# Kernel optimization log

Measured on AMD Instinct MI355X. Metric: run time of the kernel, lower is better.

Reference implementation:

```python
import jax, jax.numpy as jnp
import numpy as np

B, S, IN, OUT = 16, 512, 512, 256
D, H, L, DFF = 1024, 16, 6, 2048
HD = D // H
SCALE = HD ** -0.5
HID = 256  # fc1/fc2 hidden size


def setup_inputs() -> dict:
    key = jax.random.key(0)
    ks = jax.random.split(key, 40)
    g = lambda i, shape, s=0.02: (jax.random.normal(ks[i], shape, jnp.float32) * s)
    z = lambda shape: jnp.zeros(shape, jnp.float32)
    o = lambda shape: jnp.ones(shape, jnp.float32)
    vec = jnp.zeros((B, S), jnp.int32).at[:, 0].set(1)  # one-hot rows (assert-only arg)
    return {
        "x": jax.random.normal(ks[0], (B, S, IN), jnp.float32),
        "xm": jax.random.uniform(ks[1], (B, S), jnp.float32),
        "vecSelector": vec,
        "proj_w": g(2, (IN, D)), "proj_b": z((D,)),
        "pos": g(3, (S, D)),
        "qw": g(4, (L, D, D)), "qb": z((L, D)),
        "kw": g(5, (L, D, D)), "kb": z((L, D)),
        "vw": g(6, (L, D, D)), "vb": z((L, D)),
        "ow": g(7, (L, D, D)), "ob": z((L, D)),
        "ln1_g": o((L, D)), "ln1_b": z((L, D)),
        "ln2_g": o((L, D)), "ln2_b": z((L, D)),
        "w1": g(8, (L, D, DFF)), "b1": z((L, DFF)),
        "w2": g(9, (L, DFF, D)), "b2": z((L, D)),
        "fc1_w": g(10, (D, HID)), "fc1_b": z((HID,)),
        "fc2_w": g(11, (HID, HID)), "fc2_b": z((HID,)),
        "fc3_w": g(12, (HID, OUT)), "fc3_b": z((OUT,)),
    }


def _ln(x, g, b, eps=1e-5):
    m = jnp.mean(x, -1, keepdims=True)
    v = jnp.mean((x - m) ** 2, -1, keepdims=True)
    return (x - m) * jax.lax.rsqrt(v + eps) * g + b


def reference(x, xm, vecSelector, proj_w, proj_b, pos, qw, qb, kw, kb, vw, vb,
              ow, ob, ln1_g, ln1_b, ln2_g, ln2_b, w1, b1, w2, b2,
              fc1_w, fc1_b, fc2_w, fc2_b, fc3_w, fc3_b):
    # linear_proj + positional encoding (pos[:, :d_model] == pos)
    h = x @ proj_w + proj_b + pos  # (B,S,D)
    # key padding mask: whole batch rows masked where xm.sum(-1)==0
    skpm = jnp.broadcast_to((jnp.sum(xm, -1) == 0)[:, None], (B, S))  # (B,S) bool
    neg_inf = jnp.float32(-jnp.inf)
    for i in range(L):
        q = (h @ qw[i] + qb[i]) * SCALE
        k = h @ kw[i] + kb[i]
        v = h @ vw[i] + vb[i]
        q = q.reshape(B, S, H, HD)
        k = k.reshape(B, S, H, HD)
        v = v.reshape(B, S, H, HD)
        sc = jnp.einsum('bthd,bshd->bhts', q, k)  # (B,H,T,S)
        sc = jnp.where(skpm[:, None, None, :], neg_inf, sc)
        # safe_softmax: clamp to [-10,10] THEN softmax (-inf -> -10)
        aw = jax.nn.softmax(jnp.clip(sc, -10.0, 10.0), axis=-1)
        ao = jnp.einsum('bhts,bshd->bthd', aw, v).reshape(B, S, D)
        ao = ao @ ow[i] + ob[i]
        # forward hook: clamp + softmax over embed dim
        ao = jax.nn.softmax(jnp.clip(ao, -10.0, 10.0), axis=-1)
        # torch _sa_block's `[0]` slices batch dim of the raw tensor -> (S,D),
        # broadcast-added to every batch row
        sa = ao[0]
        h = _ln(h + sa[None, :, :], ln1_g[i], ln1_b[i])
        ff = jax.nn.relu(h @ w1[i] + b1[i]) @ w2[i] + b2[i]
        h = _ln(h + ff, ln2_g[i], ln2_b[i])
    out = h @ fc1_w + fc1_b
    for _ in range(5):
        out = out @ fc2_w + fc2_b
    out = out @ fc3_w + fc3_b  # (B,S,OUT)
    return out
```

## Files before the change

### kernel.cpp

```cpp
#include <hip/hip_runtime.h>
#include <hip/hip_bf16.h>

using bf16 = __hip_bfloat16;
typedef __attribute__((ext_vector_type(8))) short short8v;
typedef __attribute__((ext_vector_type(4))) float floatx4;

constexpr int Bc = 16, Sc = 512, INc = 512, OUTc = 256;
constexpr int Dc = 1024, Hc = 16, Lc = 6, DFFc = 2048, HIDc = 256;
constexpr float SCALEc = 0.125f;
constexpr int QKVS = 3072;
constexpr size_t LSLOT = 8388608;

__device__ inline ushort f2b(float f) {
    union { float f; unsigned u; } v; v.f = f;
    unsigned r = (v.u + 0x7FFF + ((v.u >> 16) & 1)) >> 16;
    return (ushort)r;
}
__device__ inline float b2f(ushort b) {
    union { unsigned u; float f; } v; v.u = ((unsigned)b) << 16;
    return v.f;
}
__device__ inline float ldf(const float* p) { return *p; }
__device__ inline float ldf(const ushort* p) { return b2f(*p); }

__device__ inline void gll16(const ushort* g, ushort* l) {
    __builtin_amdgcn_global_load_lds(
        (const __attribute__((address_space(1))) unsigned int*)g,
        (__attribute__((address_space(3))) unsigned int*)l, 16, 0, 0);
}

__device__ inline float blockSum256(float v) {
    __shared__ float tmp[4];
#pragma unroll
    for (int o = 32; o > 0; o >>= 1) v += __shfl_xor(v, o, 64);
    int w = threadIdx.x >> 6;
    __syncthreads();
    if ((threadIdx.x & 63) == 0) tmp[w] = v;
    __syncthreads();
    return tmp[0] + tmp[1] + tmp[2] + tmp[3];
}
__device__ inline float blockMax256(float v) {
    __shared__ float tmp[4];
#pragma unroll
    for (int o = 32; o > 0; o >>= 1) v = fmaxf(v, __shfl_xor(v, o, 64));
    int w = threadIdx.x >> 6;
    __syncthreads();
    if ((threadIdx.x & 63) == 0) tmp[w] = v;
    __syncthreads();
    return fmaxf(fmaxf(tmp[0], tmp[1]), fmaxf(tmp[2], tmp[3]));
}

__global__ __launch_bounds__(256) void mask_k(const float* __restrict__ xm, float* __restrict__ flag) {
    float s = xm[threadIdx.x] + xm[threadIdx.x + 256];
    s = blockSum256(s);
    if (threadIdx.x == 0) flag[0] = (s == 0.f) ? 1.f : 0.f;
}

__global__ __launch_bounds__(256) void transp_k(const float* __restrict__ W, ushort* __restrict__ Wt,
                                                int K, int N, float wscale) {
    __shared__ float Ls[64][65];
    const int t = threadIdx.x;
    const int n0 = blockIdx.x * 64, k0 = blockIdx.y * 64;
    const int kr = t >> 4, n4 = (t & 15) * 4;
#pragma unroll
    for (int p = 0; p < 4; ++p) {
        float4 v = *(const float4*)&W[(size_t)(k0 + kr + p * 16) * N + n0 + n4];
        Ls[kr + p * 16][n4 + 0] = v.x; Ls[kr + p * 16][n4 + 1] = v.y;
        Ls[kr + p * 16][n4 + 2] = v.z; Ls[kr + p * 16][n4 + 3] = v.w;
    }
    __syncthreads();
    const int nr = t >> 4, k4 = (t & 15) * 4;
#pragma unroll
    for (int p = 0; p < 4; ++p) {
        ushort4 o;
        o.x = f2b(Ls[k4 + 0][nr + p * 16] * wscale); o.y = f2b(Ls[k4 + 1][nr + p * 16] * wscale);
        o.z = f2b(Ls[k4 + 2][nr + p * 16] * wscale); o.w = f2b(Ls[k4 + 3][nr + p * 16] * wscale);
        *(ushort4*)&Wt[(size_t)(n0 + nr + p * 16) * K + k0 + k4] = o;
    }
}

__global__ __launch_bounds__(256) void transpall_k(
    const float* __restrict__ qw, const float* __restrict__ kw, const float* __restrict__ vw,
    const float* __restrict__ ow, const float* __restrict__ w1, const float* __restrict__ w2,
    ushort* __restrict__ Wt, int l0, size_t lstride)
{
    const int l = l0 + blockIdx.y;
    ushort* slot = Wt + (size_t)blockIdx.y * lstride;
    const int id = blockIdx.x;
    int m, tx, ty;
    if (id < 1024)      { m = id >> 8; int r = id & 255;  tx = r & 15; ty = r >> 4; }
    else if (id < 1536) { m = 4;       int r = id - 1024; tx = r & 31; ty = r >> 5; }
    else                { m = 5;       int r = id - 1536; tx = r & 15; ty = r >> 4; }
    const float* W; ushort* dst; int K, N; float wscale = 1.f;
    switch (m) {
        case 0: W = qw + (size_t)l * Dc * Dc; K = Dc; N = Dc; dst = slot; wscale = SCALEc; break;
        case 1: W = kw + (size_t)l * Dc * Dc; K = Dc; N = Dc; dst = slot + 1048576; break;
        case 2: W = vw + (size_t)l * Dc * Dc; K = Dc; N = Dc; dst = slot + 2097152; break;
        case 3: W = ow + (size_t)l * Dc * Dc; K = Dc; N = Dc; dst = slot + 3145728; break;
        case 4: W = w1 + (size_t)l * Dc * DFFc; K = Dc; N = DFFc; dst = slot + 4194304; break;
        default: W = w2 + (size_t)l * DFFc * Dc; K = DFFc; N = Dc; dst = slot + 6291456; break;
    }
    __shared__ float Ls[64][65];
    const int t = threadIdx.x;
    const int n0 = tx * 64, k0 = ty * 64;
    const int kr = t >> 4, n4 = (t & 15) * 4;
#pragma unroll
    for (int p = 0; p < 4; ++p) {
        float4 v = *(const float4*)&W[(size_t)(k0 + kr + p * 16) * N + n0 + n4];
        Ls[kr + p * 16][n4 + 0] = v.x; Ls[kr + p * 16][n4 + 1] = v.y;
        Ls[kr + p * 16][n4 + 2] = v.z; Ls[kr + p * 16][n4 + 3] = v.w;
    }
    __syncthreads();
#pragma unroll
    for (int p = 0; p < 2; ++p) {
        const int idx = t + 256 * p;
        const int n = idx >> 3, kc = (idx & 7) * 8;
        __align__(16) ushort tmp[8];
#pragma unroll
        for (int u = 0; u < 8; ++u) tmp[u] = f2b(Ls[kc + u][n] * wscale);
        *(short8v*)&dst[(size_t)(n0 + n) * K + k0 + kc] = *(short8v*)tmp;
    }
}

__device__ inline void ld16(const float* s, ushort* d) {
#pragma unroll
    for (int i = 0; i < 4; ++i) {
        float4 v = *(const float4*)(s + i * 4);
        d[i * 4 + 0] = f2b(v.x); d[i * 4 + 1] = f2b(v.y);
        d[i * 4 + 2] = f2b(v.z); d[i * 4 + 3] = f2b(v.w);
    }
}

template <typename TA, int ACT, bool ADDPOS, int OMODE>
__global__ __launch_bounds__(256) void mgemm_k(
    const TA* __restrict__ A, const ushort* __restrict__ Bt,
    const float* __restrict__ bias, const float* __restrict__ pos,
    float* __restrict__ Cf, ushort* __restrict__ Cb,
    int M, int N, int K, float scale)
{
    __shared__ __align__(16) ushort As[128 * 64];
    __shared__ __align__(16) ushort Bs[128 * 64];
    const int tid = threadIdx.x;
    const int nx = gridDim.x;
    const int nwg = nx * gridDim.y;
    int d = blockIdx.x + blockIdx.y * nx;
    if ((nwg & 7) == 0) d = (d & 7) * (nwg >> 3) + (d >> 3);
    const int m0 = (d / nx) * 128, n0 = (d % nx) * 128;
    const int lane = tid & 63, wv = tid >> 6;
    const int wm = (wv >> 1) * 64, wn = (wv & 1) * 64;
    floatx4 acc[4][4] = {};

    const int rA8 = lane >> 3, cch = lane & 7;
    const int srow = tid >> 2, scg = tid & 3;

    for (int k0 = 0; k0 < K; k0 += 64) {
#pragma unroll
        for (int p = 0; p < 4; ++p) {
            const int r = wv * 32 + p * 8 + rA8;
            const int cs = (cch ^ (r & 7)) * 8;
            gll16(&Bt[(size_t)(n0 + r) * K + k0 + cs], &Bs[(wv * 32 + p * 8) * 64]);
        }
        if constexpr (sizeof(TA) == 2) {
#pragma unroll
            for (int p = 0; p < 4; ++p) {
                const int r = wv * 32 + p * 8 + rA8;
                const int cs = (cch ^ (r & 7)) * 8;
                gll16((const ushort*)&A[(size_t)(m0 + r) * K + k0 + cs], &As[(wv * 32 + p * 8) * 64]);
            }
        } else {
#pragma unroll
            for (int p = 0; p < 2; ++p) {
                const int r = srow + p * 64;
                __align__(16) ushort ta[16];
                ld16(&A[(size_t)(m0 + r) * K + k0 + scg * 16], ta);
                const int base = r * 64, sw = (r & 7) * 8;
                *(short8v*)&As[base + ((scg * 16 + 0) ^ sw)] = *(short8v*)&ta[0];
                *(short8v*)&As[base + ((scg * 16 + 8) ^ sw)] = *(short8v*)&ta[8];
            }
        }
        __syncthreads();
#pragma unroll
        for (int s = 0; s < 2; ++s) {
            short8v af[4], bf_[4];
            const int kg = s * 32 + (lane >> 4) * 8;
#pragma unroll
            for (int f = 0; f < 4; ++f) {
                const int ra = wm + f * 16 + (lane & 15);
                af[f] = *(const short8v*)&As[ra * 64 + (kg ^ ((ra & 7) * 8))];
                const int rb = wn + f * 16 + (lane & 15);
                bf_[f] = *(const short8v*)&Bs[rb * 64 + (kg ^ ((rb & 7) * 8))];
            }
#pragma unroll
            for (int i = 0; i < 4; ++i)
#pragma unroll
                for (int j = 0; j < 4; ++j)
                    acc[i][j] = __builtin_amdgcn_mfma_f32_16x16x32_bf16(af[i], bf_[j], acc[i][j], 0, 0, 0);
        }
        __syncthreads();
    }

    const int cc = lane & 15, rr4 = (lane >> 4) * 4;
#pragma unroll
    for (int i = 0; i < 4; ++i) {
#pragma unroll
        for (int j = 0; j < 4; ++j) {
            const int col = n0 + wn + j * 16 + cc;
            const float bsv = bias[col];
#pragma unroll
            for (int q = 0; q < 4; ++q) {
                const int row = m0 + wm + i * 16 + rr4 + q;
                float v = acc[i][j][q] + bsv;
                if (ADDPOS) v += pos[(size_t)(row & (Sc - 1)) * N + col];
                v *= scale;
                if (ACT == 1) v = fmaxf(v, 0.f);
                if (OMODE == 0) Cf[(size_t)row * N + col] = v;
                else if (OMODE == 1) Cb[(size_t)row * N + col] = f2b(v);
                else { Cf[(size_t)row * N + col] = v; Cb[(size_t)row * N + col] = f2b(v); }
            }
        }
    }
}

#define SG256(ts, g) do { \
    if ((ts) < NT) { \
        const int sb_ = (ts) & 1; \
        const int kk_ = (ts) << 6; \
        _Pragma("unroll") \
        for (int ii_ = 0; ii_ < 2; ++ii_) { \
            const int ib_ = wv * 16 + ii_ * 8; \
            if ((g) == 0 || (g) == 2) { \
                const int r0_ = (ib_ < 64 ? ib_ : ib_ + 64) + (((g) == 2) ? 64 : 0); \
                const int rr_ = r0_ + rA8; \
                gll16(A + (size_t)(m0 + rr_) * K + kk_ + ((cch ^ (rr_ & 7)) << 3), \
                      &Al[sb_][r0_ * 64]); \
            } else { \
                const int r0_ = ((ib_ >> 5) * 64) + (ib_ & 31) + (((g) == 3) ? 32 : 0); \
                const int rr_ = r0_ + rA8; \
                gll16(Bt + (size_t)(n0 + rr_) * K + kk_ + ((cch ^ (rr_ & 7)) << 3), \
                      &Bl[sb_][r0_ * 64]); \
            } \
        } \
    } } while (0)

#define LDA256(bb, fb) \
    _Pragma("unroll") for (int f_ = 0; f_ < 4; ++f_) { \
        const int ra_ = wm + ((fb) + f_) * 16 + (lane & 15); \
        const int sw_ = (ra_ & 7) * 8; \
        af[f_][0] = *(const short8v*)&Al[bb][ra_ * 64 + ((kgl) ^ sw_)]; \
        af[f_][1] = *(const short8v*)&Al[bb][ra_ * 64 + ((32 + kgl) ^ sw_)]; }

#define LDB256(bb, jb) \
    _Pragma("unroll") for (int f_ = 0; f_ < 2; ++f_) { \
        const int rb_ = wn + ((jb) + f_) * 16 + (lane & 15); \
        const int sw_ = (rb_ & 7) * 8; \
        bf_[(jb) + f_][0] = *(const short8v*)&Bl[bb][rb_ * 64 + ((kgl) ^ sw_)]; \
        bf_[(jb) + f_][1] = *(const short8v*)&Bl[bb][rb_ * 64 + ((32 + kgl) ^ sw_)]; }

#define MM256(ib, jb) \
    __builtin_amdgcn_s_setprio(1); \
    _Pragma("unroll") for (int i_ = 0; i_ < 4; ++i_) \
    _Pragma("unroll") for (int j_ = 0; j_ < 2; ++j_) \
    _Pragma("unroll") for (int s_ = 0; s_ < 2; ++s_) \
        acc[(ib) + i_][(jb) + j_] = __builtin_amdgcn_mfma_f32_16x16x32_bf16( \
            af[i_][s_], bf_[(jb) + j_][s_], acc[(ib) + i_][(jb) + j_], 0, 0, 0); \
    __builtin_amdgcn_s_setprio(0);

__global__ __launch_bounds__(512) void mgemm256_k(
    const ushort* __restrict__ A, const ushort* __restrict__ Bt,
    const float* __restrict__ bias, ushort* __restrict__ Cb,
    int M, int N, int K, int ACT)
{
    __shared__ __align__(16) ushort Al[2][256 * 64];
    __shared__ __align__(16) ushort Bl[2][256 * 64];
    const int tid = threadIdx.x;
    const int lane = tid & 63, wv = tid >> 6;
    const int nx = gridDim.x, nwg = nx * gridDim.y;
    int d = blockIdx.x + blockIdx.y * nx;
    if ((nwg & 7) == 0) d = (d & 7) * (nwg >> 3) + (d >> 3);
    const int m0 = (d / nx) * 256, n0 = (d % nx) * 256;
    const int wm = (wv >> 2) * 128, wn = (wv & 3) * 64;
    const int rA8 = lane >> 3, cch = lane & 7;
    const int kgl = (lane >> 4) * 8;
    const int NT = K >> 6;
    floatx4 acc[8][4] = {};
    short8v af[4][2], bf_[4][2];

    SG256(0, 0); SG256(0, 1); SG256(0, 2); SG256(0, 3);
    SG256(1, 0); SG256(1, 1); SG256(1, 2);
    asm volatile("s_waitcnt vmcnt(6)" ::: "memory");
    __builtin_amdgcn_s_barrier();

    for (int t = 0; t < NT; ++t) {
        const int bb = t & 1;
        if (t + 1 < NT) { asm volatile("s_waitcnt vmcnt(6)" ::: "memory"); }
        else            { asm volatile("s_waitcnt vmcnt(0)" ::: "memory"); }
        LDA256(bb, 0); LDB256(bb, 0);
        SG256(t + 1, 3);
        __builtin_amdgcn_s_barrier();
        MM256(0, 0);
        __builtin_amdgcn_s_barrier();
        LDB256(bb, 2);
        SG256(t + 2, 0);
        __builtin_amdgcn_s_barrier();
        MM256(0, 2);
        __builtin_amdgcn_s_barrier();
        LDA256(bb, 4);
        SG256(t + 2, 1);
        __builtin_amdgcn_s_barrier();
        MM256(4, 0);
        __builtin_amdgcn_s_barrier();
        SG256(t + 2, 2);
        __builtin_amdgcn_s_barrier();
        MM256(4, 2);
        __builtin_amdgcn_s_barrier();
    }

    const int cc = lane & 15, rr4 = (lane >> 4) * 4;
#pragma unroll
    for (int i = 0; i < 8; ++i) {
#pragma unroll
        for (int j = 0; j < 4; ++j) {
            const int col = n0 + wn + j * 16 + cc;
            const float bsv = bias[col];
#pragma unroll
            for (int q = 0; q < 4; ++q) {
                const int row = m0 + wm + i * 16 + rr4 + q;
                float v = acc[i][j][q] + bsv;
                if (ACT) v = fmaxf(v, 0.f);
                Cb[(size_t)row * N + col] = f2b(v);
            }
        }
    }
}

__global__ __launch_bounds__(256) void fattn_k(
    const ushort* __restrict__ qkv, ushort* __restrict__ ao, const float* __restrict__ flag)
{
    const int hh = blockIdx.y;
    const int t0 = blockIdx.x * 16;
    __shared__ __align__(16) ushort Qs[16 * 64];
    __shared__ __align__(16) ushort Ks[64 * 64];
    __shared__ float Vs[64][68];
    __shared__ float Ps[16][68];
    __shared__ float rs[4][16];
    const int tid = threadIdx.x;
    const int lane = tid & 63, wv = tid >> 6;
    const bool msk = flag[0] > 0.5f;

    if (tid < 128) {
        const int r = tid >> 3, c = tid & 7;
        short8v q = *(const short8v*)&qkv[(size_t)(t0 + r) * QKVS + hh * 64 + c * 8];
        *(short8v*)&Qs[r * 64 + ((c * 8) ^ ((r & 7) * 8))] = q;
    }
    if (tid < 64) ((float*)rs)[tid] = 0.f;

    float o[4] = {};
    const int pq = tid >> 4, pd = (tid & 15) * 4;

    for (int s0 = 0; s0 < Sc; s0 += 64) {
        __syncthreads();
        {
            const int vr = tid >> 2, vc = (tid & 3) * 16;
            const ushort* vsrc = &qkv[(size_t)(s0 + vr) * QKVS + 2048 + hh * 64 + vc];
            short8v v0 = *(const short8v*)vsrc, v1 = *(const short8v*)(vsrc + 8);
#pragma unroll
            for (int u = 0; u < 8; ++u) {
                Vs[vr][vc + u] = b2f((ushort)v0[u]);
                Vs[vr][vc + 8 + u] = b2f((ushort)v1[u]);
            }
#pragma unroll
            for (int u = 0; u < 2; ++u) {
                const int task = tid + u * 256;
                const int kr = task >> 3, kc = task & 7;
                short8v kvv = *(const short8v*)&qkv[(size_t)(s0 + kr) * QKVS + 1024 + hh * 64 + kc * 8];
                *(short8v*)&Ks[kr * 64 + ((kc * 8) ^ ((kr & 7) * 8))] = kvv;
            }
        }
        __syncthreads();
        floatx4 pacc = {};
#pragma unroll
        for (int s = 0; s < 2; ++s) {
            const int kg = s * 32 + (lane >> 4) * 8;
            const int ra = lane & 15;
            short8v aq = *(const short8v*)&Qs[ra * 64 + (kg ^ ((ra & 7) * 8))];
            const int rb = 16 * wv + (lane & 15);
            short8v bk = *(const short8v*)&Ks[rb * 64 + (kg ^ ((rb & 7) * 8))];
            pacc = __builtin_amdgcn_mfma_f32_16x16x32_bf16(aq, bk, pacc, 0, 0, 0);
        }
        const int cc = lane & 15, rr4 = (lane >> 4) * 4;
#pragma unroll
        for (int q = 0; q < 4; ++q) {
            float v = fminf(fmaxf(pacc[q], -10.f), 10.f);
            if (msk) v = -10.f;
            float e = __expf(v - 10.f);
            Ps[rr4 + q][wv * 16 + cc] = e;
            float rsum = e;
            rsum += __shfl_xor(rsum, 1, 64);
            rsum += __shfl_xor(rsum, 2, 64);
            rsum += __shfl_xor(rsum, 4, 64);
            rsum += __shfl_xor(rsum, 8, 64);
            if (cc == 0) rs[wv][rr4 + q] += rsum;
        }
        __syncthreads();
#pragma unroll 8
        for (int ss = 0; ss < 64; ++ss) {
            float p = Ps[pq][ss];
#pragma unroll
            for (int u = 0; u < 4; ++u) o[u] += p * Vs[ss][pd + u];
        }
    }
    __syncthreads();
    float inv = 1.f / (rs[0][pq] + rs[1][pq] + rs[2][pq] + rs[3][pq]);
#pragma unroll
    for (int u = 0; u < 4; ++u)
        ao[(size_t)(t0 + pq) * Dc + hh * 64 + pd + u] = f2b(o[u] * inv);
}

template <typename TA, int ACT, bool ADDPOS, bool OUT_BF16, bool HASB>
__global__ __launch_bounds__(256) void gemm_k(
    const TA* __restrict__ A, const float* __restrict__ W,
    const float* __restrict__ bias, const float* __restrict__ pos,
    float* __restrict__ Cf, bf16* __restrict__ Cb,
    int M, int N, int K, float scale)
{
    __shared__ float As[16][68];
    __shared__ float Ws[16][68];
    const int tid = threadIdx.x;
    const int m0 = blockIdx.y * 64, n0 = blockIdx.x * 64;
    const int ty = tid >> 4, tx = tid & 15;
    float c[4][4] = {};

    const int ka = tid & 15, mb = tid >> 4;
    const int nw = tid & 63, kb = tid >> 6;

    for (int k0 = 0; k0 < K; k0 += 16) {
#pragma unroll
        for (int j = 0; j < 4; ++j) {
            int m = mb + 16 * j;
            As[ka][m] = ldf(&A[(size_t)(m0 + m) * K + k0 + ka]);
        }
#pragma unroll
        for (int j = 0; j < 4; ++j) {
            int k = kb + 4 * j;
            Ws[k][nw] = W[(size_t)(k0 + k) * N + n0 + nw];
        }
        __syncthreads();
#pragma unroll
        for (int k = 0; k < 16; ++k) {
            float4 av = *(const float4*)&As[k][ty * 4];
            float4 wv = *(const float4*)&Ws[k][tx * 4];
            float a[4] = {av.x, av.y, av.z, av.w};
            float w[4] = {wv.x, wv.y, wv.z, wv.w};
#pragma unroll
            for (int i = 0; i < 4; ++i)
#pragma unroll
                for (int j = 0; j < 4; ++j) c[i][j] += a[i] * w[j];
        }
        __syncthreads();
    }

#pragma unroll
    for (int i = 0; i < 4; ++i) {
        int m = m0 + ty * 4 + i;
#pragma unroll
        for (int j = 0; j < 4; ++j) {
            int n = n0 + tx * 4 + j;
            float v = c[i][j] + (HASB ? bias[n] : 0.f);
            if (ADDPOS) v += pos[(size_t)(m & (Sc - 1)) * N + n];
            v *= scale;
            if (ACT == 1) v = fmaxf(v, 0.f);
            if (OUT_BF16) Cb[(size_t)m * N + n] = __float2bfloat16(v);
            else          Cf[(size_t)m * N + n] = v;
        }
    }
}

__global__ __launch_bounds__(256) void biaschain_k(
    const float* __restrict__ fc1b, const float* __restrict__ fc2w, const float* __restrict__ fc2b,
    const float* __restrict__ fc3w, const float* __restrict__ fc3b, float* __restrict__ bc)
{
    __shared__ float vs[256];
    const int t = threadIdx.x;
    float v = fc1b[t];
    for (int r = 0; r < 5; ++r) {
        vs[t] = v; __syncthreads();
        float s = fc2b[t];
#pragma unroll 8
        for (int k = 0; k < 256; ++k) s += vs[k] * fc2w[k * 256 + t];
        v = s; __syncthreads();
    }
    vs[t] = v; __syncthreads();
    float s = fc3b[t];
#pragma unroll 8
    for (int k = 0; k < 256; ++k) s += vs[k] * fc3w[k * 256 + t];
    bc[t] = s;
}

__global__ __launch_bounds__(256) void qkvbiasall_k(
    const float* __restrict__ qb, const float* __restrict__ kb, const float* __restrict__ vb,
    float* __restrict__ o)
{
    int i = blockIdx.x * 256 + threadIdx.x;
    int l = i / QKVS, j = i - l * QKVS;
    float v = (j < 1024) ? qb[l * Dc + j] * SCALEc
            : (j < 2048) ? kb[l * Dc + j - 1024] : vb[l * Dc + j - 2048];
    o[i] = v;
}

__global__ __launch_bounds__(256) void smaddln_k(
    ushort* __restrict__ hb, const float* __restrict__ obv,
    const float* __restrict__ g, const float* __restrict__ b)
{
    const int row = blockIdx.x;
    const float* op = obv + (size_t)(row & (Sc - 1)) * Dc;
    ushort* hp = hb + (size_t)row * Dc;
    const int c0 = threadIdx.x * 4;
    float4 ov = *(const float4*)&op[c0];
    float r[4] = {ov.x, ov.y, ov.z, ov.w};
    float mx = -1e30f;
#pragma unroll
    for (int j = 0; j < 4; ++j) { r[j] = fminf(fmaxf(r[j], -10.f), 10.f); mx = fmaxf(mx, r[j]); }
    mx = blockMax256(mx);
    float s = 0.f;
#pragma unroll
    for (int j = 0; j < 4; ++j) { r[j] = __expf(r[j] - mx); s += r[j]; }
    s = blockSum256(s);
    float sinv = 1.f / s;
    ushort4 hv = *(const ushort4*)&hp[c0];
    float x[4] = {b2f(hv.x), b2f(hv.y), b2f(hv.z), b2f(hv.w)};
    float ssum = 0.f;
#pragma unroll
    for (int j = 0; j < 4; ++j) { x[j] += r[j] * sinv; ssum += x[j]; }
    float mean = blockSum256(ssum) * (1.f / (float)Dc);
    float vsum = 0.f;
#pragma unroll
    for (int j = 0; j < 4; ++j) { float d_ = x[j] - mean; vsum += d_ * d_; }
    float var = blockSum256(vsum) * (1.f / (float)Dc);
    float inv = rsqrtf(var + 1e-5f);
    float4 gv = *(const float4*)&g[c0];
    float4 bv = *(const float4*)&b[c0];
    ushort4 o4;
    o4.x = f2b((x[0] - mean) * inv * gv.x + bv.x);
    o4.y = f2b((x[1] - mean) * inv * gv.y + bv.y);
    o4.z = f2b((x[2] - mean) * inv * gv.z + bv.z);
    o4.w = f2b((x[3] - mean) * inv * gv.w + bv.w);
    *(ushort4*)&hp[c0] = o4;
}

template <bool BCAST, typename TADD>
__global__ __launch_bounds__(256) void add_ln_k(
    ushort* __restrict__ hb, const TADD* __restrict__ add,
    const float* __restrict__ g, const float* __restrict__ b)
{
    const int row = blockIdx.x;
    const TADD* ap = BCAST ? add + (size_t)(row & (Sc - 1)) * Dc : add + (size_t)row * Dc;
    ushort* hp = hb + (size_t)row * Dc;
    const int c0 = threadIdx.x * 4;
    ushort4 hv = *(const ushort4*)&hp[c0];
    float x[4] = {b2f(hv.x), b2f(hv.y), b2f(hv.z), b2f(hv.w)};
#pragma unroll
    for (int j = 0; j < 4; ++j) x[j] += ldf(&ap[c0 + j]);
    float s = x[0] + x[1] + x[2] + x[3];
    float mean = blockSum256(s) * (1.f / (float)Dc);
    float vsum = 0.f;
#pragma unroll
    for (int j = 0; j < 4; ++j) { float d = x[j] - mean; vsum += d * d; }
    float var = blockSum256(vsum) * (1.f / (float)Dc);
    float inv = rsqrtf(var + 1e-5f);
    float4 gv = *(const float4*)&g[c0];
    float4 bv = *(const float4*)&b[c0];
    ushort4 ov;
    ov.x = f2b((x[0] - mean) * inv * gv.x + bv.x);
    ov.y = f2b((x[1] - mean) * inv * gv.y + bv.y);
    ov.z = f2b((x[2] - mean) * inv * gv.z + bv.z);
    ov.w = f2b((x[3] - mean) * inv * gv.w + bv.w);
    *(ushort4*)&hp[c0] = ov;
}

extern "C" void kernel_launch(void* const* d_in, const int* in_sizes, int n_in,
                              void* d_out, int out_size, void* d_ws, size_t ws_size,
                              hipStream_t stream)
{
    const float* x      = (const float*)d_in[0];
    const float* xm     = (const float*)d_in[1];
    const float* proj_w = (const float*)d_in[3];
    const float* proj_b = (const float*)d_in[4];
    const float* pos    = (const float*)d_in[5];
    const float* qw     = (const float*)d_in[6];
    const float* qb     = (const float*)d_in[7];
    const float* kw     = (const float*)d_in[8];
    const float* kb     = (const float*)d_in[9];
    const float* vw     = (const float*)d_in[10];
    const float* vb     = (const float*)d_in[11];
    const float* ow     = (const float*)d_in[12];
    const float* obias  = (const float*)d_in[13];
    const float* ln1g   = (const float*)d_in[14];
    const float* ln1b   = (const float*)d_in[15];
    const float* ln2g   = (const float*)d_in[16];
    const float* ln2b   = (const float*)d_in[17];
    const float* w1     = (const float*)d_in[18];
    const float* b1     = (const float*)d_in[19];
    const float* w2     = (const float*)d_in[20];
    const float* b2     = (const float*)d_in[21];
    const float* fc1w   = (const float*)d_in[22];
    const float* fc1b   = (const float*)d_in[23];
    const float* fc2w   = (const float*)d_in[24];
    const float* fc2b   = (const float*)d_in[25];
    const float* fc3w   = (const float*)d_in[26];
    const float* fc3b   = (const float*)d_in[27];

    float* ws = (float*)d_ws;
    const size_t HSZ = (size_t)Bc * Sc * Dc;
    ushort* hb  = (ushort*)ws;
    ushort* ffu = (ushort*)(ws + HSZ / 2);
    float*  rgA = ws + HSZ;
    float*  meta = ws + 2 * HSZ;
    float*  flag = meta;
    float*  qkvball = meta + 256;
    ushort* Wt = (ushort*)(ws + 2 * HSZ + 262144);

    const bool big = ws_size >= (size_t)163 * 1024 * 1024;
    const size_t lstride = big ? LSLOT : 0;
    ushort* projWt = big ? Wt + (size_t)6 * LSLOT : Wt;

    ushort* qkvfu = (ushort*)rgA;
    ushort* aovu  = (ushort*)(rgA + 786432);
    float*  obv   = rgA + 1048576;
    ushort* midu  = (ushort*)rgA;
    float* W2  = rgA;
    float* W4  = rgA + 65536;
    float* W5  = rgA + 131072;
    float* C1  = rgA + 196608;
    float* Wc  = rgA + 458752;
    float* bcv = rgA + 720896;

    const int MR = Bc * Sc;

    mask_k<<<1, 256, 0, stream>>>(xm, flag);
    qkvbiasall_k<<<72, 256, 0, stream>>>(qb, kb, vb, qkvball);
    if (big)
        transpall_k<<<dim3(2048, 6), 256, 0, stream>>>(qw, kw, vw, ow, w1, w2, Wt, 0, lstride);

    transp_k<<<dim3(Dc / 64, INc / 64), 256, 0, stream>>>(proj_w, projWt, INc, Dc, 1.f);
    mgemm_k<float, 0, true, 1><<<dim3(Dc / 128, MR / 128), 256, 0, stream>>>(
        x, projWt, proj_b, pos, nullptr, hb, MR, Dc, INc, 1.f);

    for (int l = 0; l < Lc; ++l) {
        ushort* slot = Wt + (size_t)(big ? l : 0) * LSLOT;
        const float* ob_l = obias + l * Dc;
        const float* b1_l = b1 + l * DFFc;
        const float* b2_l = b2 + l * Dc;

        if (!big)
            transpall_k<<<dim3(2048, 1), 256, 0, stream>>>(qw, kw, vw, ow, w1, w2, Wt, l, 0);

        mgemm_k<ushort, 0, false, 1><<<dim3(QKVS / 128, Sc / 128), 256, 0, stream>>>(
            hb, slot, qkvball + l * QKVS, nullptr, nullptr, qkvfu, Sc, QKVS, Dc, 1.f);
        fattn_k<<<dim3(Sc / 16, Hc), 256, 0, stream>>>(qkvfu, aovu, flag);
        mgemm_k<ushort, 0, false, 0><<<dim3(Dc / 128, Sc / 128), 256, 0, stream>>>(
            aovu, slot + 3145728, ob_l, nullptr, obv, nullptr, Sc, Dc, Dc, 1.f);
        smaddln_k<<<MR, 256, 0, stream>>>(hb, obv, ln1g + l * Dc, ln1b + l * Dc);

        mgemm256_k<<<dim3(DFFc / 256, MR / 256), 512, 0, stream>>>(
            hb, slot + 4194304, b1_l, midu, MR, DFFc, Dc, 1);
        mgemm256_k<<<dim3(Dc / 256, MR / 256), 512, 0, stream>>>(
            midu, slot + 6291456, b2_l, ffu, MR, Dc, DFFc, 0);
        add_ln_k<false, ushort><<<MR, 256, 0, stream>>>(hb, ffu, ln2g + l * Dc, ln2b + l * Dc);
    }

    gemm_k<float, 0, false, false, false><<<dim3(4, 4), 256, 0, stream>>>(
        fc2w, fc2w, nullptr, nullptr, W2, nullptr, HIDc, HIDc, HIDc, 1.f);
    gemm_k<float, 0, false, false, false><<<dim3(4, 4), 256, 0, stream>>>(
        W2, W2, nullptr, nullptr, W4, nullptr, HIDc, HIDc, HIDc, 1.f);
    gemm_k<float, 0, false, false, false><<<dim3(4, 4), 256, 0, stream>>>(
        W4, fc2w, nullptr, nullptr, W5, nullptr, HIDc, HIDc, HIDc, 1.f);
    gemm_k<float, 0, false, false, false><<<dim3(4, 16), 256, 0, stream>>>(
        fc1w, W5, nullptr, nullptr, C1, nullptr, Dc, HIDc, HIDc, 1.f);
    gemm_k<float, 0, false, false, false><<<dim3(4, 16), 256, 0, stream>>>(
        C1, fc3w, nullptr, nullptr, Wc, nullptr, Dc, HIDc, HIDc, 1.f);
    biaschain_k<<<1, 256, 0, stream>>>(fc1b, fc2w, fc2b, fc3w, fc3b, bcv);
    transp_k<<<dim3(HIDc / 64, Dc / 64), 256, 0, stream>>>(Wc, Wt, Dc, HIDc, 1.f);
    mgemm_k<ushort, 0, false, 0><<<dim3(HIDc / 128, MR / 128), 256, 0, stream>>>(
        hb, Wt, bcv, nullptr, (float*)d_out, nullptr, MR, HIDc, Dc, 1.f);
}
```

Before: 1.412 ms.

## Use 64x64 GEMM tiles for small-M layers and pre-convert input to bf16

Adds a 64x64-tile MFMA GEMM and uses it for the per-layer QKV and output projections (M=512) and the final head GEMM. Smaller tiles give more workgroups on these under-filled problems. The FFN down-projection moves from the 256-tile kernel to the 128-tile kernel, again to raise the workgroup count. The fp32 input x is converted to bf16 in a separate pass so the projection GEMM can use direct global-to-LDS loads. Smaller tiles reuse less data per load, and the conversion pass adds extra memory traffic.

```diff
diff --git a/kernel.cpp b/kernel.cpp
--- a/kernel.cpp
+++ b/kernel.cpp
@@ -54,6 +54,19 @@
     float s = xm[threadIdx.x] + xm[threadIdx.x + 256];
     s = blockSum256(s);
     if (threadIdx.x == 0) flag[0] = (s == 0.f) ? 1.f : 0.f;
+}
+
+__global__ __launch_bounds__(256) void cvtx_k(const float* __restrict__ x, ushort* __restrict__ xb) {
+    const size_t i = ((size_t)blockIdx.x * 256 + threadIdx.x) * 16;
+    __align__(16) ushort o[16];
+#pragma unroll
+    for (int u = 0; u < 4; ++u) {
+        float4 v = *(const float4*)&x[i + u * 4];
+        o[u * 4 + 0] = f2b(v.x); o[u * 4 + 1] = f2b(v.y);
+        o[u * 4 + 2] = f2b(v.z); o[u * 4 + 3] = f2b(v.w);
+    }
+    *(short8v*)&xb[i] = *(short8v*)&o[0];
+    *(short8v*)&xb[i + 8] = *(short8v*)&o[8];
 }
 
 __global__ __launch_bounds__(256) void transp_k(const float* __restrict__ W, ushort* __restrict__ Wt,
@@ -122,18 +135,9 @@
     }
 }
 
-__device__ inline void ld16(const float* s, ushort* d) {
-#pragma unroll
-    for (int i = 0; i < 4; ++i) {
-        float4 v = *(const float4*)(s + i * 4);
-        d[i * 4 + 0] = f2b(v.x); d[i * 4 + 1] = f2b(v.y);
-        d[i * 4 + 2] = f2b(v.z); d[i * 4 + 3] = f2b(v.w);
-    }
-}
-
-template <typename TA, int ACT, bool ADDPOS, int OMODE>
+template <int ACT, bool ADDPOS, int OMODE>
 __global__ __launch_bounds__(256) void mgemm_k(
-    const TA* __restrict__ A, const ushort* __restrict__ Bt,
+    const ushort* __restrict__ A, const ushort* __restrict__ Bt,
     const float* __restrict__ bias, const float* __restrict__ pos,
     float* __restrict__ Cf, ushort* __restrict__ Cb,
     int M, int N, int K, float scale)
@@ -151,7 +155,6 @@
     floatx4 acc[4][4] = {};
 
     const int rA8 = lane >> 3, cch = lane & 7;
-    const int srow = tid >> 2, scg = tid & 3;
 
     for (int k0 = 0; k0 < K; k0 += 64) {
 #pragma unroll
@@ -159,24 +162,7 @@
             const int r = wv * 32 + p * 8 + rA8;
             const int cs = (cch ^ (r & 7)) * 8;
             gll16(&Bt[(size_t)(n0 + r) * K + k0 + cs], &Bs[(wv * 32 + p * 8) * 64]);
-        }
-        if constexpr (sizeof(TA) == 2) {
-#pragma unroll
-            for (int p = 0; p < 4; ++p) {
-                const int r = wv * 32 + p * 8 + rA8;
-                const int cs = (cch ^ (r & 7)) * 8;
-                gll16((const ushort*)&A[(size_t)(m0 + r) * K + k0 + cs], &As[(wv * 32 + p * 8) * 64]);
-            }
-        } else {
-#pragma unroll
-            for (int p = 0; p < 2; ++p) {
-                const int r = srow + p * 64;
-                __align__(16) ushort ta[16];
-                ld16(&A[(size_t)(m0 + r) * K + k0 + scg * 16], ta);
-                const int base = r * 64, sw = (r & 7) * 8;
-                *(short8v*)&As[base + ((scg * 16 + 0) ^ sw)] = *(short8v*)&ta[0];
-                *(short8v*)&As[base + ((scg * 16 + 8) ^ sw)] = *(short8v*)&ta[8];
-            }
+            gll16(&A[(size_t)(m0 + r) * K + k0 + cs], &As[(wv * 32 + p * 8) * 64]);
         }
         __syncthreads();
 #pragma unroll
@@ -217,6 +203,65 @@
                 else if (OMODE == 1) Cb[(size_t)row * N + col] = f2b(v);
                 else { Cf[(size_t)row * N + col] = v; Cb[(size_t)row * N + col] = f2b(v); }
             }
+        }
+    }
+}
+
+template <int OMODE>
+__global__ __launch_bounds__(256) void mgemm64_k(
+    const ushort* __restrict__ A, const ushort* __restrict__ Bt,
+    const float* __restrict__ bias,
+    float* __restrict__ Cf, ushort* __restrict__ Cb,
+    int M, int N, int K)
+{
+    __shared__ __align__(16) ushort As[64 * 64];
+    __shared__ __align__(16) ushort Bs[64 * 64];
+    const int tid = threadIdx.x;
+    const int nx = gridDim.x;
+    const int nwg = nx * gridDim.y;
+    int d = blockIdx.x + blockIdx.y * nx;
+    if ((nwg & 7) == 0) d = (d & 7) * (nwg >> 3) + (d >> 3);
+    const int m0 = (d / nx) * 64, n0 = (d % nx) * 64;
+    const int lane = tid & 63, wv = tid >> 6;
+    floatx4 acc[4] = {};
+
+    const int rA8 = lane >> 3, cch = lane & 7;
+
+    for (int k0 = 0; k0 < K; k0 += 64) {
+#pragma unroll
+        for (int p = 0; p < 2; ++p) {
+            const int r = wv * 16 + p * 8 + rA8;
+            const int cs = (cch ^ (r & 7)) * 8;
+            gll16(&A[(size_t)(m0 + r) * K + k0 + cs], &As[(wv * 16 + p * 8) * 64]);
+            gll16(&Bt[(size_t)(n0 + r) * K + k0 + cs], &Bs[(wv * 16 + p * 8) * 64]);
+        }
+        __syncthreads();
+#pragma unroll
+        for (int s = 0; s < 2; ++s) {
+            const int kg = s * 32 + (lane >> 4) * 8;
+            const int rb = wv * 16 + (lane & 15);
+            short8v bf_ = *(const short8v*)&Bs[rb * 64 + (kg ^ ((rb & 7) * 8))];
+#pragma unroll
+            for (int f = 0; f < 4; ++f) {
+                const int ra = f * 16 + (lane & 15);
+                short8v af = *(const short8v*)&As[ra * 64 + (kg ^ ((ra & 7) * 8))];
+                acc[f] = __builtin_amdgcn_mfma_f32_16x16x32_bf16(af, bf_, acc[f], 0, 0, 0);
+            }
+        }
+        __syncthreads();
+    }
+
+    const int cc = lane & 15, rr4 = (lane >> 4) * 4;
+    const int col = n0 + wv * 16 + cc;
+    const float bsv = bias[col];
+#pragma unroll
+    for (int f = 0; f < 4; ++f) {
+#pragma unroll
+        for (int q = 0; q < 4; ++q) {
+            const int row = m0 + f * 16 + rr4 + q;
+            float v = acc[f][q] + bsv;
+            if (OMODE == 0) Cf[(size_t)row * N + col] = v;
+            else            Cb[(size_t)row * N + col] = f2b(v);
         }
     }
 }
@@ -416,10 +461,10 @@
         ao[(size_t)(t0 + pq) * Dc + hh * 64 + pd + u] = f2b(o[u] * inv);
 }
 
-template <typename TA, int ACT, bool ADDPOS, bool OUT_BF16, bool HASB>
+template <int ACT, bool OUT_BF16, bool HASB>
 __global__ __launch_bounds__(256) void gemm_k(
-    const TA* __restrict__ A, const float* __restrict__ W,
-    const float* __restrict__ bias, const float* __restrict__ pos,
+    const float* __restrict__ A, const float* __restrict__ W,
+    const float* __restrict__ bias,
     float* __restrict__ Cf, bf16* __restrict__ Cb,
     int M, int N, int K, float scale)
 {
@@ -437,7 +482,7 @@
 #pragma unroll
         for (int j = 0; j < 4; ++j) {
             int m = mb + 16 * j;
-            As[ka][m] = ldf(&A[(size_t)(m0 + m) * K + k0 + ka]);
+            As[ka][m] = A[(size_t)(m0 + m) * K + k0 + ka];
         }
 #pragma unroll
         for (int j = 0; j < 4; ++j) {
@@ -466,7 +511,6 @@
         for (int j = 0; j < 4; ++j) {
             int n = n0 + tx * 4 + j;
             float v = c[i][j] + (HASB ? bias[n] : 0.f);
-            if (ADDPOS) v += pos[(size_t)(m & (Sc - 1)) * N + n];
             v *= scale;
             if (ACT == 1) v = fmaxf(v, 0.f);
             if (OUT_BF16) Cb[(size_t)m * N + n] = __float2bfloat16(v);
@@ -547,13 +591,12 @@
     *(ushort4*)&hp[c0] = o4;
 }
 
-template <bool BCAST, typename TADD>
 __global__ __launch_bounds__(256) void add_ln_k(
-    ushort* __restrict__ hb, const TADD* __restrict__ add,
+    ushort* __restrict__ hb, const ushort* __restrict__ add,
     const float* __restrict__ g, const float* __restrict__ b)
 {
     const int row = blockIdx.x;
-    const TADD* ap = BCAST ? add + (size_t)(row & (Sc - 1)) * Dc : add + (size_t)row * Dc;
+    const ushort* ap = add + (size_t)row * Dc;
     ushort* hp = hb + (size_t)row * Dc;
     const int c0 = threadIdx.x * 4;
     ushort4 hv = *(const ushort4*)&hp[c0];
@@ -627,6 +670,7 @@
     ushort* aovu  = (ushort*)(rgA + 786432);
     float*  obv   = rgA + 1048576;
     ushort* midu  = (ushort*)rgA;
+    ushort* xb    = (ushort*)rgA;
     float* W2  = rgA;
     float* W4  = rgA + 65536;
     float* W5  = rgA + 131072;
@@ -641,9 +685,10 @@
     if (big)
         transpall_k<<<dim3(2048, 6), 256, 0, stream>>>(qw, kw, vw, ow, w1, w2, Wt, 0, lstride);
 
+    cvtx_k<<<(MR * INc) / (256 * 16), 256, 0, stream>>>(x, xb);
     transp_k<<<dim3(Dc / 64, INc / 64), 256, 0, stream>>>(proj_w, projWt, INc, Dc, 1.f);
-    mgemm_k<float, 0, true, 1><<<dim3(Dc / 128, MR / 128), 256, 0, stream>>>(
-        x, projWt, proj_b, pos, nullptr, hb, MR, Dc, INc, 1.f);
+    mgemm_k<0, true, 1><<<dim3(Dc / 128, MR / 128), 256, 0, stream>>>(
+        xb, projWt, proj_b, pos, nullptr, hb, MR, Dc, INc, 1.f);
 
     for (int l = 0; l < Lc; ++l) {
         ushort* slot = Wt + (size_t)(big ? l : 0) * LSLOT;
@@ -654,32 +699,32 @@
         if (!big)
             transpall_k<<<dim3(2048, 1), 256, 0, stream>>>(qw, kw, vw, ow, w1, w2, Wt, l, 0);
 
-        mgemm_k<ushort, 0, false, 1><<<dim3(QKVS / 128, Sc / 128), 256, 0, stream>>>(
-            hb, slot, qkvball + l * QKVS, nullptr, nullptr, qkvfu, Sc, QKVS, Dc, 1.f);
+        mgemm64_k<1><<<dim3(QKVS / 64, Sc / 64), 256, 0, stream>>>(
+            hb, slot, qkvball + l * QKVS, nullptr, qkvfu, Sc, QKVS, Dc);
         fattn_k<<<dim3(Sc / 16, Hc), 256, 0, stream>>>(qkvfu, aovu, flag);
-        mgemm_k<ushort, 0, false, 0><<<dim3(Dc / 128, Sc / 128), 256, 0, stream>>>(
-            aovu, slot + 3145728, ob_l, nullptr, obv, nullptr, Sc, Dc, Dc, 1.f);
+        mgemm64_k<0><<<dim3(Dc / 64, Sc / 64), 256, 0, stream>>>(
+            aovu, slot + 3145728, ob_l, obv, nullptr, Sc, Dc, Dc);
         smaddln_k<<<MR, 256, 0, stream>>>(hb, obv, ln1g + l * Dc, ln1b + l * Dc);
 
         mgemm256_k<<<dim3(DFFc / 256, MR / 256), 512, 0, stream>>>(
             hb, slot + 4194304, b1_l, midu, MR, DFFc, Dc, 1);
-        mgemm256_k<<<dim3(Dc / 256, MR / 256), 512, 0, stream>>>(
-            midu, slot + 6291456, b2_l, ffu, MR, Dc, DFFc, 0);
-        add_ln_k<false, ushort><<<MR, 256, 0, stream>>>(hb, ffu, ln2g + l * Dc, ln2b + l * Dc);
-    }
-
-    gemm_k<float, 0, false, false, false><<<dim3(4, 4), 256, 0, stream>>>(
-        fc2w, fc2w, nullptr, nullptr, W2, nullptr, HIDc, HIDc, HIDc, 1.f);
-    gemm_k<float, 0, false, false, false><<<dim3(4, 4), 256, 0, stream>>>(
-        W2, W2, nullptr, nullptr, W4, nullptr, HIDc, HIDc, HIDc, 1.f);
-    gemm_k<float, 0, false, false, false><<<dim3(4, 4), 256, 0, stream>>>(
-        W4, fc2w, nullptr, nullptr, W5, nullptr, HIDc, HIDc, HIDc, 1.f);
-    gemm_k<float, 0, false, false, false><<<dim3(4, 16), 256, 0, stream>>>(
-        fc1w, W5, nullptr, nullptr, C1, nullptr, Dc, HIDc, HIDc, 1.f);
-    gemm_k<float, 0, false, false, false><<<dim3(4, 16), 256, 0, stream>>>(
-        C1, fc3w, nullptr, nullptr, Wc, nullptr, Dc, HIDc, HIDc, 1.f);
+        mgemm_k<0, false, 1><<<dim3(Dc / 128, MR / 128), 256, 0, stream>>>(
+            midu, slot + 6291456, b2_l, nullptr, nullptr, ffu, MR, Dc, DFFc, 1.f);
+        add_ln_k<<<MR, 256, 0, stream>>>(hb, ffu, ln2g + l * Dc, ln2b + l * Dc);
+    }
+
+    gemm_k<0, false, false><<<dim3(4, 4), 256, 0, stream>>>(
+        fc2w, fc2w, nullptr, W2, nullptr, HIDc, HIDc, HIDc, 1.f);
+    gemm_k<0, false, false><<<dim3(4, 4), 256, 0, stream>>>(
+        W2, W2, nullptr, W4, nullptr, HIDc, HIDc, HIDc, 1.f);
+    gemm_k<0, false, false><<<dim3(4, 4), 256, 0, stream>>>(
+        W4, fc2w, nullptr, W5, nullptr, HIDc, HIDc, HIDc, 1.f);
+    gemm_k<0, false, false><<<dim3(4, 16), 256, 0, stream>>>(
+        fc1w, W5, nullptr, C1, nullptr, Dc, HIDc, HIDc, 1.f);
+    gemm_k<0, false, false><<<dim3(4, 16), 256, 0, stream>>>(
+        C1, fc3w, nullptr, Wc, nullptr, Dc, HIDc, HIDc, 1.f);
     biaschain_k<<<1, 256, 0, stream>>>(fc1b, fc2w, fc2b, fc3w, fc3b, bcv);
     transp_k<<<dim3(HIDc / 64, Dc / 64), 256, 0, stream>>>(Wc, Wt, Dc, HIDc, 1.f);
-    mgemm_k<ushort, 0, false, 0><<<dim3(HIDc / 128, MR / 128), 256, 0, stream>>>(
-        hb, Wt, bcv, nullptr, (float*)d_out, nullptr, MR, HIDc, Dc, 1.f);
-}
+    mgemm64_k<0><<<dim3(HIDc / 64, MR / 64), 256, 0, stream>>>(
+        hb, Wt, bcv, (float*)d_out, nullptr, MR, HIDc, Dc);
+}
```

Result: faster. 1.215 ms (median of 3 runs) (-13.9%).
